# Optimization experiments

Measured on AMD Instinct MI355X. Metric: run time of the kernel, lower is better.

The kernel has to match this reference:

```python
import jax, jax.numpy as jnp
import numpy as np

N_GRAPHS = 256
STEPS = 3


def setup_inputs() -> dict:
    key = jax.random.key(0)
    ks = jax.random.split(key, 8)
    N, d, out = 100000, 512, 256
    s = 0.05
    x = jax.random.normal(ks[0], (N, d), dtype=jnp.float32)
    batch = jnp.sort(jax.random.randint(ks[1], (N,), 0, N_GRAPHS)).astype(jnp.int64)
    W_ih = jax.random.normal(ks[2], (4 * d, 2 * d), dtype=jnp.float32) * s
    W_hh = jax.random.normal(ks[3], (4 * d, d), dtype=jnp.float32) * s
    b_ih = jax.random.normal(ks[4], (4 * d,), dtype=jnp.float32) * s
    b_hh = jax.random.normal(ks[5], (4 * d,), dtype=jnp.float32) * s
    W_proj = jax.random.normal(ks[6], (out, 2 * d), dtype=jnp.float32) * s
    b_proj = jax.random.normal(ks[7], (out,), dtype=jnp.float32) * s
    return {"x": x, "batch": batch, "W_ih": W_ih, "W_hh": W_hh,
            "b_ih": b_ih, "b_hh": b_hh, "W_proj": W_proj, "b_proj": b_proj}


def _set2set(x, batch, W_ih, W_hh, b_ih, b_hh):
    N, d = x.shape
    B = N_GRAPHS
    h = jnp.zeros((B, d), x.dtype)
    c = jnp.zeros((B, d), x.dtype)
    q_star = jnp.zeros((B, 2 * d), x.dtype)
    for _ in range(STEPS):
        # single-step LSTM cell (PyTorch gate order i,f,g,o)
        gates = q_star @ W_ih.T + b_ih + h @ W_hh.T + b_hh
        i, f, g, o = jnp.split(gates, 4, axis=-1)
        c = jax.nn.sigmoid(f) * c + jax.nn.sigmoid(i) * jnp.tanh(g)
        h = jax.nn.sigmoid(o) * jnp.tanh(c)
        q = h                                   # [B, d]
        # segment softmax attention over nodes
        e = jnp.sum(x * q[batch], axis=-1)      # [N]
        m = jax.ops.segment_max(e, batch, num_segments=B)
        m = jnp.where(jnp.isfinite(m), m, 0.0)  # guard empty segments
        ex = jnp.exp(e - m[batch])
        denom = jax.ops.segment_sum(ex, batch, num_segments=B) + 1e-16
        a = ex / denom[batch]                   # [N]
        r = jax.ops.segment_sum(a[:, None] * x, batch, num_segments=B)  # [B, d]
        q_star = jnp.concatenate([q, r], axis=-1)
    return q_star


def reference(x, batch, W_ih, W_hh, b_ih, b_hh, W_proj, b_proj):
    pooled = _set2set(x, batch, W_ih, W_hh, b_ih, b_hh)  # [B, 2d]
    return pooled @ W_proj.T + b_proj                    # [B, out]
```

## Files before the change

### kernel.cpp

```cpp
#include <hip/hip_runtime.h>
#include <hip/hip_bf16.h>


typedef __bf16 bf16_t;
typedef __bf16 bf16x8 __attribute__((ext_vector_type(8)));
typedef float  f32x4  __attribute__((ext_vector_type(4)));

#define D     512
#define B_GR  256
#define FOURD 2048
#define KCAT  1536
#define AWAVES 16
#define DET_BLOCKS 400

__global__ void detect_part1(const int* __restrict__ b32, int N,
                             const unsigned short* __restrict__ xh,
                             int* __restrict__ partA, int* __restrict__ partB) {
    __shared__ int sA, sB;
    if (threadIdx.x == 0) { sA = 0; sB = 0; }
    __syncthreads();
    int gid = blockIdx.x * blockDim.x + threadIdx.x;
    int stride = gridDim.x * blockDim.x;
    int dec = 0;
    for (int i = gid; i < N - 1; i += stride)
        if (b32[i] > b32[i + 1]) dec = 1;
    int bad = 0;
    for (int i = gid; i < 1024; i += stride) {
        unsigned e = (xh[i] >> 7) & 0xff;
        if (e >= 134) bad = 1;
    }
    if (dec) atomicOr(&sA, 1);
    if (bad) atomicOr(&sB, 1);
    __syncthreads();
    if (threadIdx.x == 0) { partA[blockIdx.x] = sA; partB[blockIdx.x] = sB; }
}

__global__ void detect_part2(const int* __restrict__ partA,
                             const int* __restrict__ partB, int nblk,
                             int* __restrict__ flags) {
    __shared__ int sA, sB;
    if (threadIdx.x == 0) { sA = 0; sB = 0; }
    __syncthreads();
    int a = 0, b = 0;
    for (int i = threadIdx.x; i < nblk; i += blockDim.x) {
        a |= partA[i];
        b |= partB[i];
    }
    if (a) atomicOr(&sA, 1);
    if (b) atomicOr(&sB, 1);
    __syncthreads();
    if (threadIdx.x == 0) { flags[0] = sA; flags[1] = sB; }
}

__global__ void seg_bounds_kernel(const void* __restrict__ batch, int N, int B,
                                  const int* __restrict__ flags,
                                  int* __restrict__ seg) {
    int n = blockIdx.x * blockDim.x + threadIdx.x;
    if (n >= N) return;
    const int is64 = flags[0];
    const int* b32 = (const int*)batch;
    const long long* b64 = (const long long*)batch;
    int cur = is64 ? (int)b64[n] : b32[n];
    if (n == 0) {
        for (int b = 0; b <= cur && b <= B; ++b) seg[b] = 0;
    } else {
        int prev = is64 ? (int)b64[n - 1] : b32[n - 1];
        for (int b = prev + 1; b <= cur && b <= B; ++b) seg[b] = n;
    }
    if (n == N - 1) {
        for (int b = cur + 1; b <= B; ++b) seg[b] = N;
    }
}

__device__ __forceinline__ bf16x8 load_frag(const void* base, int ld, int row,
                                            int k, int f32) {
    if (f32) {
        const float* p = (const float*)base + (size_t)row * ld + k;
        bf16x8 r;
#pragma unroll
        for (int j = 0; j < 8; ++j) r[j] = (bf16_t)p[j];
        return r;
    }
    return *(const bf16x8*)((const bf16_t*)base + (size_t)row * ld + k);
}

__device__ __forceinline__ float load_bias(const void* b, int i, int f32) {
    return f32 ? ((const float*)b)[i] : (float)((const bf16_t*)b)[i];
}

__global__ __launch_bounds__(64)
void gemm_bt(const bf16_t* __restrict__ A, int lda,
             const void* __restrict__ B1, int ldb1,
             const void* __restrict__ B2, int ldb2, int ksplit, int K,
             const void* __restrict__ bias1, const void* __restrict__ bias2,
             float* __restrict__ Cf, bf16_t* __restrict__ Cb, int ldc,
             const int* __restrict__ flags) {
    const int f32w  = flags[1];
    const int lane  = threadIdx.x;
    const int n0    = blockIdx.x * 16;
    const int m0    = blockIdx.y * 16;
    const int rowA  = m0 + (lane & 15);
    const int rowB  = n0 + (lane & 15);
    const int kbase = (lane >> 4) * 8;

    f32x4 acc = {0.f, 0.f, 0.f, 0.f};

    const int k1 = (ksplit < K) ? ksplit : K;
    for (int k0 = 0; k0 < k1; k0 += 32) {
        int k = k0 + kbase;
        bf16x8 a = *(const bf16x8*)(A + (size_t)rowA * lda + k);
        bf16x8 b = load_frag(B1, ldb1, rowB, k, f32w);
        acc = __builtin_amdgcn_mfma_f32_16x16x32_bf16(a, b, acc, 0, 0, 0);
    }
    for (int k0 = k1; k0 < K; k0 += 32) {
        int k = k0 + kbase;
        bf16x8 a = *(const bf16x8*)(A + (size_t)rowA * lda + k);
        bf16x8 b = load_frag(B2, ldb2, rowB, k - ksplit, f32w);
        acc = __builtin_amdgcn_mfma_f32_16x16x32_bf16(a, b, acc, 0, 0, 0);
    }

    const int col   = lane & 15;
    const int rbase = (lane >> 4) * 4;
    float bias = 0.f;
    if (bias1) bias += load_bias(bias1, n0 + col, f32w);
    if (bias2) bias += load_bias(bias2, n0 + col, f32w);
    const bool out_f32 = Cf && (Cb == nullptr || f32w);
#pragma unroll
    for (int r = 0; r < 4; ++r) {
        int m = m0 + rbase + r;
        int n = n0 + col;
        float v = acc[r] + bias;
        if (out_f32) Cf[(size_t)m * ldc + n] = v;
        else         Cb[(size_t)m * ldc + n] = (bf16_t)v;
    }
}

__global__ void lstm_cell(const float* __restrict__ gates,
                          float* __restrict__ c, float* __restrict__ h,
                          bf16_t* __restrict__ Abuf,
                          const void* __restrict__ b_ih,
                          const void* __restrict__ b_hh,
                          const int* __restrict__ flags, int first) {
    int idx = blockIdx.x * blockDim.x + threadIdx.x;
    int b = idx >> 9, t = idx & 511;
    float gi, gf, gg, go, cv;
    if (first) {
        const int f32w = flags[1];
        gi = load_bias(b_ih, t,        f32w) + load_bias(b_hh, t,        f32w);
        gf = load_bias(b_ih, 512 + t,  f32w) + load_bias(b_hh, 512 + t,  f32w);
        gg = load_bias(b_ih, 1024 + t, f32w) + load_bias(b_hh, 1024 + t, f32w);
        go = load_bias(b_ih, 1536 + t, f32w) + load_bias(b_hh, 1536 + t, f32w);
        cv = 0.f;
    } else {
        const float* g = gates + (size_t)b * FOURD;
        gi = g[t]; gf = g[512 + t]; gg = g[1024 + t]; go = g[1536 + t];
        cv = c[idx];
    }
    float si = 1.f / (1.f + __expf(-gi));
    float sf = 1.f / (1.f + __expf(-gf));
    float so = 1.f / (1.f + __expf(-go));
    float tg = tanhf(gg);
    float cn = sf * cv + si * tg;
    float hn = so * tanhf(cn);
    c[idx] = cn;
    h[idx] = hn;
    bf16_t hb = (bf16_t)hn;
    Abuf[(size_t)b * KCAT + t]        = hb;
    Abuf[(size_t)b * KCAT + 1024 + t] = hb;
}

__global__ __launch_bounds__(1024)
void attention_kernel(const void* __restrict__ xv_, int N,
                      const int* __restrict__ seg,
                      const float* __restrict__ hbuf,
                      bf16_t* __restrict__ Abuf,
                      const int* __restrict__ flags) {
    __shared__ float racc2[AWAVES][D];
    __shared__ float red_m[AWAVES], red_s[AWAVES];

    const int f32x = flags[1];
    const int b    = blockIdx.x;
    int s  = seg[b];
    int en = seg[b + 1];
    s  = (s  < 0) ? 0 : ((s  > N) ? N : s);
    en = (en < s) ? s : ((en > N) ? N : en);
    const int cnt  = en - s;
    const int tid  = threadIdx.x;
    const int wave = tid >> 6;
    const int lane = tid & 63;

    float hl[8];
    {
        const float* hp = hbuf + ((size_t)b << 9) + lane * 8;
#pragma unroll
        for (int j = 0; j < 8; ++j) hl[j] = hp[j];
    }

    float m_w = -INFINITY, s_w = 0.f;
    float r_w[8];
#pragma unroll
    for (int j = 0; j < 8; ++j) r_w[j] = 0.f;

    for (int i = wave; i < cnt; i += AWAVES) {
        int n = s + i;
        float xf[8];
        if (f32x) {
            const float* xp = (const float*)xv_ + ((size_t)n << 9) + lane * 8;
            float4 v0 = *(const float4*)xp;
            float4 v1 = *(const float4*)(xp + 4);
            xf[0] = v0.x; xf[1] = v0.y; xf[2] = v0.z; xf[3] = v0.w;
            xf[4] = v1.x; xf[5] = v1.y; xf[6] = v1.z; xf[7] = v1.w;
        } else {
            bf16x8 xv = *(const bf16x8*)((const bf16_t*)xv_ + ((size_t)n << 9) + lane * 8);
#pragma unroll
            for (int j = 0; j < 8; ++j) xf[j] = (float)xv[j];
        }
        float d = 0.f;
#pragma unroll
        for (int j = 0; j < 8; ++j) d += xf[j] * hl[j];
#pragma unroll
        for (int off = 32; off > 0; off >>= 1) d += __shfl_xor(d, off, 64);
        float m_new = fmaxf(m_w, d);
        float alpha = __expf(m_w - m_new);
        float p     = __expf(d - m_new);
        s_w = s_w * alpha + p;
#pragma unroll
        for (int j = 0; j < 8; ++j) r_w[j] = r_w[j] * alpha + p * xf[j];
        m_w = m_new;
    }

    if (lane == 0) { red_m[wave] = m_w; red_s[wave] = s_w; }
    __syncthreads();

    float M = -INFINITY, S = 0.f;
#pragma unroll
    for (int w = 0; w < AWAVES; ++w)
        if (red_s[w] > 0.f) M = fmaxf(M, red_m[w]);
#pragma unroll
    for (int w = 0; w < AWAVES; ++w)
        if (red_s[w] > 0.f) S += red_s[w] * __expf(red_m[w] - M);
    float Sinv  = 1.f / (S + 1e-16f);
    float scale = (s_w > 0.f) ? __expf(m_w - M) * Sinv : 0.f;

#pragma unroll
    for (int j = 0; j < 8; ++j) racc2[wave][lane * 8 + j] = r_w[j] * scale;
    __syncthreads();

    if (tid < D) {
        float r = 0.f;
#pragma unroll
        for (int w = 0; w < AWAVES; ++w) r += racc2[w][tid];
        Abuf[(size_t)b * KCAT + 512 + tid] = (bf16_t)r;
    }
}

extern "C" void kernel_launch(void* const* d_in, const int* in_sizes, int n_in,
                              void* d_out, int out_size, void* d_ws, size_t ws_size,
                              hipStream_t stream) {
    const void* x      = d_in[0];
    const void* batch  = d_in[1];
    const void* W_ih   = d_in[2];
    const void* W_hh   = d_in[3];
    const void* b_ih   = d_in[4];
    const void* b_hh   = d_in[5];
    const void* W_proj = d_in[6];
    const void* b_proj = d_in[7];

    const int N = in_sizes[1];
    const int B = B_GR;

    char* p = (char*)d_ws;
    size_t used = 0;
    auto carve = [&](size_t bytes) {
        void* r = (void*)p;
        size_t a = (bytes + 1023) & ~(size_t)1023;
        p += a;
        used += a;
        return r;
    };
    float*  gates = (float*)carve((size_t)B * FOURD * 4);
    float*  c_buf = (float*)carve((size_t)B * D * 4);
    float*  h_buf = (float*)carve((size_t)B * D * 4);
    bf16_t* Abuf  = (bf16_t*)carve((size_t)B * KCAT * 2);
    int*    seg   = (int*)carve((size_t)(B + 1) * 4);
    int*    flags = (int*)carve(8);
    int*    partA = (int*)carve(DET_BLOCKS * 4);
    int*    partB = (int*)carve(DET_BLOCKS * 4);

    if (used > ws_size) return;

    detect_part1<<<DET_BLOCKS, 256, 0, stream>>>(
        (const int*)batch, N, (const unsigned short*)x, partA, partB);
    detect_part2<<<1, 512, 0, stream>>>(partA, partB, DET_BLOCKS, flags);
    seg_bounds_kernel<<<(N + 255) / 256, 256, 0, stream>>>(batch, N, B, flags, seg);

    lstm_cell<<<(B * D) / 256, 256, 0, stream>>>(
        nullptr, c_buf, h_buf, Abuf, b_ih, b_hh, flags, 1);
    attention_kernel<<<B, 1024, 0, stream>>>(x, N, seg, h_buf, Abuf, flags);

    for (int step = 1; step < 3; ++step) {
        gemm_bt<<<dim3(FOURD / 16, B / 16), 64, 0, stream>>>(
            Abuf, KCAT, W_ih, 1024, W_hh, 512, 1024, KCAT,
            b_ih, b_hh, gates, nullptr, FOURD, flags);

        lstm_cell<<<(B * D) / 256, 256, 0, stream>>>(
            gates, c_buf, h_buf, Abuf, b_ih, b_hh, flags, 0);

        attention_kernel<<<B, 1024, 0, stream>>>(x, N, seg, h_buf, Abuf, flags);
    }

    gemm_bt<<<dim3(256 / 16, B / 16), 64, 0, stream>>>(
        Abuf, KCAT, W_proj, 1024, nullptr, 0, 1024, 1024,
        b_proj, nullptr, (float*)d_out, (bf16_t*)d_out, 256, flags);
}
```

Baseline: 490.2 us.

## Cache bf16 copy of x, fuse LSTM cell into gate GEMM, pre-convert weights

On the first attention step the f32 node features are converted to a bf16 copy in workspace, and later steps read that copy, halving their x traffic. The LSTM cell is fused into the gate GEMM epilogue: each block computes all four gate tiles per column and writes c, h and the A buffer directly, with ping-pong A buffers. Weights and biases are concatenated and converted to bf16 once in a prep kernel. The attention loop now processes two rows per wave iteration. The costs are an extra prep pass over the weights, an extra write of a 100MB bf16 x copy, and a dependence on the workspace being large enough for that copy.

```diff
diff --git a/kernel.cpp b/kernel.cpp
--- a/kernel.cpp
+++ b/kernel.cpp
@@ -12,6 +12,10 @@
 #define KCAT  1536
 #define AWAVES 16
 #define DET_BLOCKS 400
+
+__device__ __forceinline__ float load_f(const void* b, int i, int f32) {
+    return f32 ? ((const float*)b)[i] : (float)((const bf16_t*)b)[i];
+}
 
 __global__ void detect_part1(const int* __restrict__ b32, int N,
                              const unsigned short* __restrict__ xh,
@@ -72,95 +76,51 @@
     }
 }
 
-__device__ __forceinline__ bf16x8 load_frag(const void* base, int ld, int row,
-                                            int k, int f32) {
-    if (f32) {
-        const float* p = (const float*)base + (size_t)row * ld + k;
-        bf16x8 r;
-#pragma unroll
-        for (int j = 0; j < 8; ++j) r[j] = (bf16_t)p[j];
-        return r;
-    }
-    return *(const bf16x8*)((const bf16_t*)base + (size_t)row * ld + k);
-}
-
-__device__ __forceinline__ float load_bias(const void* b, int i, int f32) {
-    return f32 ? ((const float*)b)[i] : (float)((const bf16_t*)b)[i];
-}
-
-__global__ __launch_bounds__(64)
-void gemm_bt(const bf16_t* __restrict__ A, int lda,
-             const void* __restrict__ B1, int ldb1,
-             const void* __restrict__ B2, int ldb2, int ksplit, int K,
-             const void* __restrict__ bias1, const void* __restrict__ bias2,
-             float* __restrict__ Cf, bf16_t* __restrict__ Cb, int ldc,
-             const int* __restrict__ flags) {
-    const int f32w  = flags[1];
-    const int lane  = threadIdx.x;
-    const int n0    = blockIdx.x * 16;
-    const int m0    = blockIdx.y * 16;
-    const int rowA  = m0 + (lane & 15);
-    const int rowB  = n0 + (lane & 15);
-    const int kbase = (lane >> 4) * 8;
-
-    f32x4 acc = {0.f, 0.f, 0.f, 0.f};
-
-    const int k1 = (ksplit < K) ? ksplit : K;
-    for (int k0 = 0; k0 < k1; k0 += 32) {
-        int k = k0 + kbase;
-        bf16x8 a = *(const bf16x8*)(A + (size_t)rowA * lda + k);
-        bf16x8 b = load_frag(B1, ldb1, rowB, k, f32w);
-        acc = __builtin_amdgcn_mfma_f32_16x16x32_bf16(a, b, acc, 0, 0, 0);
-    }
-    for (int k0 = k1; k0 < K; k0 += 32) {
-        int k = k0 + kbase;
-        bf16x8 a = *(const bf16x8*)(A + (size_t)rowA * lda + k);
-        bf16x8 b = load_frag(B2, ldb2, rowB, k - ksplit, f32w);
-        acc = __builtin_amdgcn_mfma_f32_16x16x32_bf16(a, b, acc, 0, 0, 0);
-    }
-
-    const int col   = lane & 15;
-    const int rbase = (lane >> 4) * 4;
-    float bias = 0.f;
-    if (bias1) bias += load_bias(bias1, n0 + col, f32w);
-    if (bias2) bias += load_bias(bias2, n0 + col, f32w);
-    const bool out_f32 = Cf && (Cb == nullptr || f32w);
-#pragma unroll
-    for (int r = 0; r < 4; ++r) {
-        int m = m0 + rbase + r;
-        int n = n0 + col;
-        float v = acc[r] + bias;
-        if (out_f32) Cf[(size_t)m * ldc + n] = v;
-        else         Cb[(size_t)m * ldc + n] = (bf16_t)v;
-    }
-}
-
-__global__ void lstm_cell(const float* __restrict__ gates,
-                          float* __restrict__ c, float* __restrict__ h,
-                          bf16_t* __restrict__ Abuf,
-                          const void* __restrict__ b_ih,
-                          const void* __restrict__ b_hh,
-                          const int* __restrict__ flags, int first) {
+#define WCAT_E (FOURD * KCAT)
+#define WP_E   (256 * 1024)
+__global__ void prep_kernel(const void* __restrict__ W_ih,
+                            const void* __restrict__ W_hh,
+                            const void* __restrict__ b_ih,
+                            const void* __restrict__ b_hh,
+                            const void* __restrict__ W_proj,
+                            const void* __restrict__ b_proj,
+                            const int* __restrict__ flags,
+                            bf16_t* __restrict__ Wcat, bf16_t* __restrict__ Wp,
+                            float* __restrict__ bsum, float* __restrict__ bp) {
+    const int f32 = flags[1];
+    int gid = blockIdx.x * blockDim.x + threadIdx.x;
+    int stride = gridDim.x * blockDim.x;
+    const int total = WCAT_E + WP_E + FOURD + 256;
+    for (int idx = gid; idx < total; idx += stride) {
+        if (idx < WCAT_E) {
+            int r = idx / KCAT, k = idx - r * KCAT;
+            float v = (k < 1024) ? load_f(W_ih, r * 1024 + k, f32)
+                                 : load_f(W_hh, r * 512 + (k - 1024), f32);
+            Wcat[idx] = (bf16_t)v;
+        } else if (idx < WCAT_E + WP_E) {
+            int j = idx - WCAT_E;
+            Wp[j] = (bf16_t)load_f(W_proj, j, f32);
+        } else if (idx < WCAT_E + WP_E + FOURD) {
+            int i = idx - WCAT_E - WP_E;
+            bsum[i] = load_f(b_ih, i, f32) + load_f(b_hh, i, f32);
+        } else {
+            int i = idx - WCAT_E - WP_E - FOURD;
+            bp[i] = load_f(b_proj, i, f32);
+        }
+    }
+}
+
+__global__ void lstm0_kernel(const float* __restrict__ bsum,
+                             float* __restrict__ c, float* __restrict__ h,
+                             bf16_t* __restrict__ Abuf) {
     int idx = blockIdx.x * blockDim.x + threadIdx.x;
     int b = idx >> 9, t = idx & 511;
-    float gi, gf, gg, go, cv;
-    if (first) {
-        const int f32w = flags[1];
-        gi = load_bias(b_ih, t,        f32w) + load_bias(b_hh, t,        f32w);
-        gf = load_bias(b_ih, 512 + t,  f32w) + load_bias(b_hh, 512 + t,  f32w);
-        gg = load_bias(b_ih, 1024 + t, f32w) + load_bias(b_hh, 1024 + t, f32w);
-        go = load_bias(b_ih, 1536 + t, f32w) + load_bias(b_hh, 1536 + t, f32w);
-        cv = 0.f;
-    } else {
-        const float* g = gates + (size_t)b * FOURD;
-        gi = g[t]; gf = g[512 + t]; gg = g[1024 + t]; go = g[1536 + t];
-        cv = c[idx];
-    }
+    float gi = bsum[t], gf = bsum[512 + t], gg = bsum[1024 + t], go = bsum[1536 + t];
+    (void)gf;
     float si = 1.f / (1.f + __expf(-gi));
-    float sf = 1.f / (1.f + __expf(-gf));
     float so = 1.f / (1.f + __expf(-go));
     float tg = tanhf(gg);
-    float cn = sf * cv + si * tg;
+    float cn = si * tg;
     float hn = so * tanhf(cn);
     c[idx] = cn;
     h[idx] = hn;
@@ -169,17 +129,85 @@
     Abuf[(size_t)b * KCAT + 1024 + t] = hb;
 }
 
+__global__ __launch_bounds__(64)
+void gemm_lstm(const bf16_t* __restrict__ AbufIn,
+               const bf16_t* __restrict__ Wcat,
+               const float* __restrict__ bsum,
+               float* __restrict__ c, float* __restrict__ h,
+               bf16_t* __restrict__ AbufOut) {
+    const int lane  = threadIdx.x;
+    const int t0    = blockIdx.x * 16;
+    const int m0    = blockIdx.y * 16;
+    const int rowA  = m0 + (lane & 15);
+    const int colB  = t0 + (lane & 15);
+    const int kbase = (lane >> 4) * 8;
+
+    f32x4 acc[4] = {{0,0,0,0},{0,0,0,0},{0,0,0,0},{0,0,0,0}};
+
+    for (int k0 = 0; k0 < KCAT; k0 += 32) {
+        int k = k0 + kbase;
+        bf16x8 a = *(const bf16x8*)(AbufIn + (size_t)rowA * KCAT + k);
+#pragma unroll
+        for (int g = 0; g < 4; ++g) {
+            bf16x8 bfr = *(const bf16x8*)(Wcat + (size_t)(g * 512 + colB) * KCAT + k);
+            acc[g] = __builtin_amdgcn_mfma_f32_16x16x32_bf16(a, bfr, acc[g], 0, 0, 0);
+        }
+    }
+
+    const int col   = colB;
+    const int rbase = (lane >> 4) * 4;
+    float bi = bsum[col], bf = bsum[512 + col], bg = bsum[1024 + col], bo = bsum[1536 + col];
+#pragma unroll
+    for (int r = 0; r < 4; ++r) {
+        int m = m0 + rbase + r;
+        float gi = acc[0][r] + bi;
+        float gf = acc[1][r] + bf;
+        float gg = acc[2][r] + bg;
+        float go = acc[3][r] + bo;
+        size_t ci = (size_t)m * D + col;
+        float cv = c[ci];
+        float si = 1.f / (1.f + __expf(-gi));
+        float sf = 1.f / (1.f + __expf(-gf));
+        float so = 1.f / (1.f + __expf(-go));
+        float tg = tanhf(gg);
+        float cn = sf * cv + si * tg;
+        float hn = so * tanhf(cn);
+        c[ci] = cn;
+        h[ci] = hn;
+        bf16_t hb = (bf16_t)hn;
+        AbufOut[(size_t)m * KCAT + col]        = hb;
+        AbufOut[(size_t)m * KCAT + 1024 + col] = hb;
+    }
+}
+
+__device__ __forceinline__ void load_row_f32(const float* xp, float* xf) {
+    float4 v0 = *(const float4*)xp;
+    float4 v1 = *(const float4*)(xp + 4);
+    xf[0] = v0.x; xf[1] = v0.y; xf[2] = v0.z; xf[3] = v0.w;
+    xf[4] = v1.x; xf[5] = v1.y; xf[6] = v1.z; xf[7] = v1.w;
+}
+__device__ __forceinline__ void load_row_bf16(const bf16_t* xp, float* xf) {
+    bf16x8 v = *(const bf16x8*)xp;
+#pragma unroll
+    for (int j = 0; j < 8; ++j) xf[j] = (float)v[j];
+}
+
 __global__ __launch_bounds__(1024)
-void attention_kernel(const void* __restrict__ xv_, int N,
+void attention_kernel(const void* __restrict__ x, bf16_t* __restrict__ xb,
+                      int use_xb, int step0, int N,
                       const int* __restrict__ seg,
                       const float* __restrict__ hbuf,
-                      bf16_t* __restrict__ Abuf,
+                      bf16_t* __restrict__ AbufOut,
                       const int* __restrict__ flags) {
     __shared__ float racc2[AWAVES][D];
     __shared__ float red_m[AWAVES], red_s[AWAVES];
 
     const int f32x = flags[1];
-    const int b    = blockIdx.x;
+    const bool rd32 = f32x && (step0 || !use_xb);
+    const void* xsrc = rd32 ? x : (f32x ? (const void*)xb : x);
+    const bool wrxb = f32x && step0 && use_xb;
+
+    const int b = blockIdx.x;
     int s  = seg[b];
     int en = seg[b + 1];
     s  = (s  < 0) ? 0 : ((s  > N) ? N : s);
@@ -201,31 +229,53 @@
 #pragma unroll
     for (int j = 0; j < 8; ++j) r_w[j] = 0.f;
 
-    for (int i = wave; i < cnt; i += AWAVES) {
-        int n = s + i;
-        float xf[8];
-        if (f32x) {
-            const float* xp = (const float*)xv_ + ((size_t)n << 9) + lane * 8;
-            float4 v0 = *(const float4*)xp;
-            float4 v1 = *(const float4*)(xp + 4);
-            xf[0] = v0.x; xf[1] = v0.y; xf[2] = v0.z; xf[3] = v0.w;
-            xf[4] = v1.x; xf[5] = v1.y; xf[6] = v1.z; xf[7] = v1.w;
+    for (int i = 2 * wave; i < cnt; i += 2 * AWAVES) {
+        int n1 = s + i;
+        bool has2 = (i + 1) < cnt;
+        float x1[8], x2[8];
+        size_t off1 = ((size_t)n1 << 9) + lane * 8;
+        size_t off2 = off1 + D;
+        if (rd32) {
+            load_row_f32((const float*)xsrc + off1, x1);
+            if (has2) load_row_f32((const float*)xsrc + off2, x2);
         } else {
-            bf16x8 xv = *(const bf16x8*)((const bf16_t*)xv_ + ((size_t)n << 9) + lane * 8);
-#pragma unroll
-            for (int j = 0; j < 8; ++j) xf[j] = (float)xv[j];
-        }
-        float d = 0.f;
-#pragma unroll
-        for (int j = 0; j < 8; ++j) d += xf[j] * hl[j];
-#pragma unroll
-        for (int off = 32; off > 0; off >>= 1) d += __shfl_xor(d, off, 64);
-        float m_new = fmaxf(m_w, d);
+            load_row_bf16((const bf16_t*)xsrc + off1, x1);
+            if (has2) load_row_bf16((const bf16_t*)xsrc + off2, x2);
+        }
+        if (!has2) {
+#pragma unroll
+            for (int j = 0; j < 8; ++j) x2[j] = 0.f;
+        }
+        if (wrxb) {
+            bf16x8 v1;
+#pragma unroll
+            for (int j = 0; j < 8; ++j) v1[j] = (bf16_t)x1[j];
+            *(bf16x8*)(xb + off1) = v1;
+            if (has2) {
+                bf16x8 v2;
+#pragma unroll
+                for (int j = 0; j < 8; ++j) v2[j] = (bf16_t)x2[j];
+                *(bf16x8*)(xb + off2) = v2;
+            }
+        }
+        float d1 = 0.f, d2 = 0.f;
+#pragma unroll
+        for (int j = 0; j < 8; ++j) { d1 += x1[j] * hl[j]; d2 += x2[j] * hl[j]; }
+#pragma unroll
+        for (int off = 32; off > 0; off >>= 1) {
+            d1 += __shfl_xor(d1, off, 64);
+            d2 += __shfl_xor(d2, off, 64);
+        }
+        if (!has2) d2 = -INFINITY;
+        float m12   = fmaxf(d1, d2);
+        float m_new = fmaxf(m_w, m12);
         float alpha = __expf(m_w - m_new);
-        float p     = __expf(d - m_new);
-        s_w = s_w * alpha + p;
-#pragma unroll
-        for (int j = 0; j < 8; ++j) r_w[j] = r_w[j] * alpha + p * xf[j];
+        float p1    = __expf(d1 - m_new);
+        float p2    = __expf(d2 - m_new);
+        s_w = s_w * alpha + p1 + p2;
+#pragma unroll
+        for (int j = 0; j < 8; ++j)
+            r_w[j] = r_w[j] * alpha + p1 * x1[j] + p2 * x2[j];
         m_w = m_new;
     }
 
@@ -250,7 +300,38 @@
         float r = 0.f;
 #pragma unroll
         for (int w = 0; w < AWAVES; ++w) r += racc2[w][tid];
-        Abuf[(size_t)b * KCAT + 512 + tid] = (bf16_t)r;
+        AbufOut[(size_t)b * KCAT + 512 + tid] = (bf16_t)r;
+    }
+}
+
+__global__ __launch_bounds__(64)
+void gemm_proj(const bf16_t* __restrict__ A,
+               const bf16_t* __restrict__ Wp, const float* __restrict__ bp,
+               void* __restrict__ out, const int* __restrict__ flags) {
+    const int f32o  = flags[1];
+    const int lane  = threadIdx.x;
+    const int n0    = blockIdx.x * 16;
+    const int m0    = blockIdx.y * 16;
+    const int rowA  = m0 + (lane & 15);
+    const int rowB  = n0 + (lane & 15);
+    const int kbase = (lane >> 4) * 8;
+
+    f32x4 acc = {0.f, 0.f, 0.f, 0.f};
+    for (int k0 = 0; k0 < 1024; k0 += 32) {
+        int k = k0 + kbase;
+        bf16x8 a = *(const bf16x8*)(A  + (size_t)rowA * KCAT + k);
+        bf16x8 b = *(const bf16x8*)(Wp + (size_t)rowB * 1024 + k);
+        acc = __builtin_amdgcn_mfma_f32_16x16x32_bf16(a, b, acc, 0, 0, 0);
+    }
+    const int col   = n0 + (lane & 15);
+    const int rbase = (lane >> 4) * 4;
+    float bias = bp[col];
+#pragma unroll
+    for (int r = 0; r < 4; ++r) {
+        int m = m0 + rbase + r;
+        float v = acc[r] + bias;
+        if (f32o) ((float*)out)[(size_t)m * 256 + col]  = v;
+        else      ((bf16_t*)out)[(size_t)m * 256 + col] = (bf16_t)v;
     }
 }
 
@@ -278,38 +359,41 @@
         used += a;
         return r;
     };
-    float*  gates = (float*)carve((size_t)B * FOURD * 4);
     float*  c_buf = (float*)carve((size_t)B * D * 4);
     float*  h_buf = (float*)carve((size_t)B * D * 4);
-    bf16_t* Abuf  = (bf16_t*)carve((size_t)B * KCAT * 2);
+    bf16_t* Abuf0 = (bf16_t*)carve((size_t)B * KCAT * 2);
+    bf16_t* Abuf1 = (bf16_t*)carve((size_t)B * KCAT * 2);
+    bf16_t* Wcat  = (bf16_t*)carve((size_t)FOURD * KCAT * 2);
+    bf16_t* Wp    = (bf16_t*)carve((size_t)256 * 1024 * 2);
+    float*  bsum  = (float*)carve((size_t)FOURD * 4);
+    float*  bp    = (float*)carve((size_t)256 * 4);
     int*    seg   = (int*)carve((size_t)(B + 1) * 4);
     int*    flags = (int*)carve(8);
     int*    partA = (int*)carve(DET_BLOCKS * 4);
     int*    partB = (int*)carve(DET_BLOCKS * 4);
-
     if (used > ws_size) return;
+    bf16_t* xb = (bf16_t*)carve((size_t)N * D * 2);
+    int use_xb = (used <= ws_size) ? 1 : 0;
 
     detect_part1<<<DET_BLOCKS, 256, 0, stream>>>(
         (const int*)batch, N, (const unsigned short*)x, partA, partB);
     detect_part2<<<1, 512, 0, stream>>>(partA, partB, DET_BLOCKS, flags);
     seg_bounds_kernel<<<(N + 255) / 256, 256, 0, stream>>>(batch, N, B, flags, seg);
-
-    lstm_cell<<<(B * D) / 256, 256, 0, stream>>>(
-        nullptr, c_buf, h_buf, Abuf, b_ih, b_hh, flags, 1);
-    attention_kernel<<<B, 1024, 0, stream>>>(x, N, seg, h_buf, Abuf, flags);
-
-    for (int step = 1; step < 3; ++step) {
-        gemm_bt<<<dim3(FOURD / 16, B / 16), 64, 0, stream>>>(
-            Abuf, KCAT, W_ih, 1024, W_hh, 512, 1024, KCAT,
-            b_ih, b_hh, gates, nullptr, FOURD, flags);
-
-        lstm_cell<<<(B * D) / 256, 256, 0, stream>>>(
-            gates, c_buf, h_buf, Abuf, b_ih, b_hh, flags, 0);
-
-        attention_kernel<<<B, 1024, 0, stream>>>(x, N, seg, h_buf, Abuf, flags);
-    }
-
-    gemm_bt<<<dim3(256 / 16, B / 16), 64, 0, stream>>>(
-        Abuf, KCAT, W_proj, 1024, nullptr, 0, 1024, 1024,
-        b_proj, nullptr, (float*)d_out, (bf16_t*)d_out, 256, flags);
-}
+    prep_kernel<<<1024, 256, 0, stream>>>(W_ih, W_hh, b_ih, b_hh, W_proj, b_proj,
+                                          flags, Wcat, Wp, bsum, bp);
+
+    lstm0_kernel<<<(B * D) / 256, 256, 0, stream>>>(bsum, c_buf, h_buf, Abuf0);
+    attention_kernel<<<B, 1024, 0, stream>>>(x, xb, use_xb, 1, N, seg,
+                                             h_buf, Abuf0, flags);
+
+    gemm_lstm<<<dim3(D / 16, B / 16), 64, 0, stream>>>(
+        Abuf0, Wcat, bsum, c_buf, h_buf, Abuf1);
+    attention_kernel<<<B, 1024, 0, stream>>>(x, xb, use_xb, 0, N, seg,
+                                             h_buf, Abuf1, flags);
+    gemm_lstm<<<dim3(D / 16, B / 16), 64, 0, stream>>>(
+        Abuf1, Wcat, bsum, c_buf, h_buf, Abuf0);
+    attention_kernel<<<B, 1024, 0, stream>>>(x, xb, use_xb, 0, N, seg,
+                                             h_buf, Abuf0, flags);
+
+    gemm_proj<<<dim3(256 / 16, B / 16), 64, 0, stream>>>(Abuf0, Wp, bp, d_out, flags);
+}
```

Measured after the change: 424.2 us. -13.5%, faster.
